# Optimization experiments

Measured on AMD Instinct MI355X. Metric: run time of the kernel, lower is better.

## Reference

```python
import jax, jax.numpy as jnp
import numpy as np

B, T, DP, DQ, DO = 128, 2048, 256, 256, 256


def setup_inputs() -> dict:
    key = jax.random.key(0)
    ks = jax.random.split(key, 10)
    return {
        "input_p": jax.random.normal(ks[0], (B, DP), dtype=jnp.float32),
        "mask_p": jnp.ones((B,), dtype=jnp.float32),
        "input_q": jax.random.normal(ks[1], (B, T, DQ), dtype=jnp.float32),
        "mask_q": jax.random.randint(ks[2], (B, T), 0, 2, dtype=jnp.int32),
        "h_tm1": jax.random.normal(ks[3], (B, DO), dtype=jnp.float32),
        # layer-0 parameters (depth == 0)
        "W_p_r": jax.random.normal(ks[4], (DO, DP + DO), dtype=jnp.float32) * 0.04,
        "b_p_r": jnp.zeros((DO,), dtype=jnp.float32),
        "W_q": jax.random.normal(ks[5], (DO, DQ), dtype=jnp.float32) * 0.05,
        "b_q": jnp.zeros((DO,), dtype=jnp.float32),
        "w": jax.random.normal(ks[6], (DO,), dtype=jnp.float32) * 0.05,
        "match_b": jnp.ones((1,), dtype=jnp.float32),
        "depth": 0,
    }


def masked_softmax(x, m, axis=-1):
    x = jnp.clip(x, -15.0, 15.0)
    x = x * m
    e_x = jnp.exp(x - jnp.max(x, axis=axis, keepdims=True))
    e_x = e_x * m
    return e_x / (jnp.sum(e_x, axis=axis, keepdims=True) + 1e-6)


def reference(input_p, mask_p, input_q, mask_q, h_tm1, W_p_r, b_p_r, W_q, b_q, w, match_b, depth):
    mq = mask_q.astype(jnp.float32)
    # G_p_r: [B, 1, DO]
    G_p_r = (jnp.concatenate([input_p, h_tm1], axis=-1) @ W_p_r.T + b_p_r)[:, None, :]
    # G_q: [B, T, DO]
    G_q = input_q @ W_q.T + b_q
    G = jnp.tanh(G_p_r + G_q)
    alpha = jnp.einsum("btd,d->bt", G, w) + match_b  # [B, T]
    alpha = masked_softmax(alpha, mq, axis=-1)
    z = jnp.einsum("bt,btd->bd", alpha, input_q)  # bmm context
    return jnp.concatenate([input_p, z], axis=1)  # [B, DP+DQ]
```

## Files before the change

### kernel.cpp

```cpp
#include <hip/hip_runtime.h>
#include <hip/hip_bf16.h>

typedef short short8 __attribute__((ext_vector_type(8)));
typedef float floatx4 __attribute__((ext_vector_type(4)));

constexpr int Bn = 128, Tn = 2048, DPn = 256, DQn = 256, DOn = 256;
constexpr int RCH = 32;
constexpr int NCH = Tn / RCH;

__device__ inline unsigned pk2(float x, float y) {
    __hip_bfloat162 h = __float22bfloat162_rn(make_float2(x, y));
    return *(unsigned*)&h;
}
__device__ inline float fast_tanh(float x) {
    float e = __expf(2.0f * x);
    return 1.0f - 2.0f / (e + 1.0f);
}

__global__ __launch_bounds__(256) void prep_kernel(const float* __restrict__ wq,
                                                   unsigned short* __restrict__ wqbf,
                                                   const float* __restrict__ input_p,
                                                   const float* __restrict__ h_tm1,
                                                   const float* __restrict__ Wpr,
                                                   const float* __restrict__ bpr,
                                                   const float* __restrict__ bq,
                                                   float* __restrict__ base) {
    __shared__ float v[512];
    __shared__ float ps[128];
    int tid = threadIdx.x;
    if (blockIdx.x < 64) {
        int idx = blockIdx.x * 256 + tid;
        float4 x = ((const float4*)wq)[idx];
        ((uint2*)wqbf)[idx] = make_uint2(pk2(x.x, x.y), pk2(x.z, x.w));
        return;
    }
    int bi = blockIdx.x - 64;
    int b = bi >> 1, half = bi & 1;
    v[tid]       = input_p[b * DPn + tid];
    v[256 + tid] = h_tm1[b * DOn + tid];
    __syncthreads();
    int dl = tid & 127, seg = tid >> 7;
    int d = half * 128 + dl;
    const float4* row = (const float4*)(Wpr + (size_t)d * 512 + seg * 256);
    const float4* vv  = (const float4*)(v + seg * 256);
    float acc = 0.f;
#pragma unroll 8
    for (int i = 0; i < 64; i++) {
        float4 r = row[i], x = vv[i];
        acc = fmaf(r.x, x.x, acc);
        acc = fmaf(r.y, x.y, acc);
        acc = fmaf(r.z, x.z, acc);
        acc = fmaf(r.w, x.w, acc);
    }
    if (seg) ps[dl] = acc;
    __syncthreads();
    if (!seg) base[b * DOn + d] = acc + ps[dl] + bpr[d] + bq[d];
}

__global__ __launch_bounds__(256, 4) void fused_kernel(const float* __restrict__ q,
                                                       const unsigned short* __restrict__ wqbf,
                                                       const float* __restrict__ base,
                                                       const float* __restrict__ wvec,
                                                       const float* __restrict__ matchb,
                                                       const int* __restrict__ maskq,
                                                       float* __restrict__ zpart,
                                                       float* __restrict__ spart,
                                                       float* __restrict__ mpart) {
    __shared__ __align__(16) float tile[RCH * 256];
    __shared__ __align__(16) float zp[4][256];
    __shared__ __align__(16) float partl[32][4];

    int b = blockIdx.y, c = blockIdx.x;
    int t0 = c * RCH;
    int tid = threadIdx.x;
    int w = tid >> 6, lane = tid & 63, l15 = lane & 15, quad = lane >> 4;
    char* tb = (char*)tile;
    float mb = matchb[0];

    {
        const float* qsrc = q + ((size_t)b * Tn + t0) * DQn;
#pragma unroll
        for (int i = 0; i < 8; i++) {
            int r = w * 8 + i;
            float4 x = *(const float4*)(qsrc + (size_t)r * DQn + lane * 4);
            *(float4*)(tb + r * 1024 + ((lane * 16) ^ ((r & 7) << 4))) = x;
        }
    }
    __syncthreads();

    short8 af[2][8];
    {
        int swz = (l15 & 7) << 4;
#pragma unroll
        for (int mt = 0; mt < 2; mt++) {
            const char* ab = tb + (mt * 16 + l15) * 1024;
#pragma unroll
            for (int ks = 0; ks < 8; ks++) {
                int cb = quad * 32 + ks * 128;
                float4 f0 = *(const float4*)(ab + (cb ^ swz));
                float4 f1 = *(const float4*)(ab + ((cb + 16) ^ swz));
                union { unsigned u[4]; short8 s; } cv;
                cv.u[0] = pk2(f0.x, f0.y);
                cv.u[1] = pk2(f0.z, f0.w);
                cv.u[2] = pk2(f1.x, f1.y);
                cv.u[3] = pk2(f1.z, f1.w);
                af[mt][ks] = cv.s;
            }
        }
    }
    float prow[2][4] = {{0.f, 0.f, 0.f, 0.f}, {0.f, 0.f, 0.f, 0.f}};
    {
        const unsigned short* bbase = wqbf + (size_t)(w * 64 + l15) * 256 + quad * 8;
#pragma unroll
        for (int nt = 0; nt < 4; nt++) {
            short8 bfr[8];
#pragma unroll
            for (int ks = 0; ks < 8; ks++)
                bfr[ks] = *(const short8*)(bbase + nt * 16 * 256 + ks * 32);
            int n = w * 64 + nt * 16 + l15;
            float bnv = base[b * DOn + n];
            float wnv = wvec[n];
#pragma unroll
            for (int mt = 0; mt < 2; mt++) {
                floatx4 acc = {0.f, 0.f, 0.f, 0.f};
#pragma unroll
                for (int ks = 0; ks < 8; ks++)
                    acc = __builtin_amdgcn_mfma_f32_16x16x32_bf16(af[mt][ks], bfr[ks], acc, 0, 0, 0);
#pragma unroll
                for (int rr = 0; rr < 4; rr++) {
                    float gg = fast_tanh(acc[rr] + bnv);
                    prow[mt][rr] = fmaf(gg, wnv, prow[mt][rr]);
                }
            }
        }
    }
#pragma unroll
    for (int off = 1; off < 16; off <<= 1)
#pragma unroll
        for (int mt = 0; mt < 2; mt++)
#pragma unroll
            for (int rr = 0; rr < 4; rr++) prow[mt][rr] += __shfl_xor(prow[mt][rr], off);
    if (l15 == 0) {
#pragma unroll
        for (int mt = 0; mt < 2; mt++)
#pragma unroll
            for (int rr = 0; rr < 4; rr++) partl[mt * 16 + quad * 4 + rr][w] = prow[mt][rr];
    }
    __syncthreads();

    float ew;
    {
        int t = lane & 31;
        float4 pl = *(const float4*)&partl[t][0];
        float lg = pl.x + pl.y + pl.z + pl.w + mb;
        float m = (float)maskq[(size_t)b * Tn + t0 + t];
        float x = fminf(fmaxf(lg, -15.f), 15.f) * m;
        ew = __expf(x - 15.f) * m;
        float xm = x, es = ew;
#pragma unroll
        for (int off = 1; off < 32; off <<= 1) {
            xm = fmaxf(xm, __shfl_xor(xm, off));
            es += __shfl_xor(es, off);
        }
        if (tid == 0) {
            mpart[b * NCH + c] = xm;
            spart[b * NCH + c] = es;
        }
    }

    {
        float a0 = 0.f, a1 = 0.f, a2 = 0.f, a3 = 0.f;
#pragma unroll
        for (int i = 0; i < 8; i++) {
            int r = w * 8 + i;
            float e = __shfl(ew, r);
            float4 x = *(const float4*)(tb + r * 1024 + ((lane * 16) ^ (i << 4)));
            a0 = fmaf(e, x.x, a0);
            a1 = fmaf(e, x.y, a1);
            a2 = fmaf(e, x.z, a2);
            a3 = fmaf(e, x.w, a3);
        }
        *(float4*)&zp[w][lane * 4] = make_float4(a0, a1, a2, a3);
    }
    __syncthreads();
    {
        float zs = zp[0][tid] + zp[1][tid] + zp[2][tid] + zp[3][tid];
        zpart[((size_t)b * NCH + c) * DQn + tid] = zs;
    }
}

__global__ __launch_bounds__(256) void final_kernel(const float* __restrict__ input_p,
                                                    const float* __restrict__ zpart,
                                                    const float* __restrict__ spart,
                                                    const float* __restrict__ mpart,
                                                    float* __restrict__ out) {
    int b = blockIdx.x, tid = threadIdx.x;
    float S = 0.f, mx = -1e30f;
#pragma unroll 8
    for (int c = 0; c < NCH; c++) {
        S += spart[b * NCH + c];
        mx = fmaxf(mx, mpart[b * NCH + c]);
    }
    float denom = S + 1e-6f * __expf(mx - 15.f);
    float inv = 1.0f / denom;
    float zs = 0.f;
#pragma unroll 8
    for (int c = 0; c < NCH; c++) zs += zpart[((size_t)b * NCH + c) * DQn + tid];
    out[(size_t)b * 512 + tid] = input_p[(size_t)b * DPn + tid];
    out[(size_t)b * 512 + 256 + tid] = zs * inv;
}

extern "C" void kernel_launch(void* const* d_in, const int* in_sizes, int n_in,
                              void* d_out, int out_size, void* d_ws, size_t ws_size,
                              hipStream_t stream) {
    const float* input_p = (const float*)d_in[0];
    const float* input_q = (const float*)d_in[2];
    const int*   mask_q  = (const int*)d_in[3];
    const float* h_tm1   = (const float*)d_in[4];
    const float* W_p_r   = (const float*)d_in[5];
    const float* b_p_r   = (const float*)d_in[6];
    const float* W_q     = (const float*)d_in[7];
    const float* b_q     = (const float*)d_in[8];
    const float* w       = (const float*)d_in[9];
    const float* match_b = (const float*)d_in[10];
    float* out = (float*)d_out;

    char* ws = (char*)d_ws;
    unsigned short* wqbf = (unsigned short*)ws;
    float* base  = (float*)(ws + 131072);
    float* zpart = (float*)(ws + 262144);
    float* spart = (float*)(ws + 262144 + 8388608);
    float* mpart = (float*)(ws + 262144 + 8388608 + 32768);

    prep_kernel<<<320, 256, 0, stream>>>(W_q, wqbf, input_p, h_tm1, W_p_r, b_p_r, b_q, base);
    fused_kernel<<<dim3(NCH, Bn), 256, 0, stream>>>(input_q, wqbf, base, w, match_b,
                                                    mask_q, zpart, spart, mpart);
    final_kernel<<<Bn, 256, 0, stream>>>(input_p, zpart, spart, mpart, out);
}
```

Baseline: 482.9 us.

## Double chunk rows, load Q tile via global_load_lds, hold W_q fragments in registers

Doubles the per-block time chunk from 32 to 64 rows, so each block keeps all 4×8 bf16 W_q fragments in registers and reuses them across four 16-row sub-tiles. The global-to-register-to-LDS copy of the Q tile is replaced by direct global_load_lds, and the MFMA operands are swapped so each lane accumulates a whole row's logit with fewer cross-lane shuffles. Partial buffers shrink because there are half as many chunks. In exchange the kernel uses more registers and LDS, occupancy drops to 2 blocks per SIMD group, and the grid has half as many blocks.

```diff
diff --git a/kernel.cpp b/kernel.cpp
--- a/kernel.cpp
+++ b/kernel.cpp
@@ -5,7 +5,7 @@
 typedef float floatx4 __attribute__((ext_vector_type(4)));
 
 constexpr int Bn = 128, Tn = 2048, DPn = 256, DQn = 256, DOn = 256;
-constexpr int RCH = 32;
+constexpr int RCH = 64;
 constexpr int NCH = Tn / RCH;
 
 __device__ inline unsigned pk2(float x, float y) {
@@ -15,6 +15,11 @@
 __device__ inline float fast_tanh(float x) {
     float e = __expf(2.0f * x);
     return 1.0f - 2.0f / (e + 1.0f);
+}
+__device__ inline void load_lds16(const void* g, void* l) {
+    __builtin_amdgcn_global_load_lds((const __attribute__((address_space(1))) unsigned int*)g,
+                                     (__attribute__((address_space(3))) unsigned int*)l,
+                                     16, 0, 0);
 }
 
 __global__ __launch_bounds__(256) void prep_kernel(const float* __restrict__ wq,
@@ -57,7 +62,7 @@
     if (!seg) base[b * DOn + d] = acc + ps[dl] + bpr[d] + bq[d];
 }
 
-__global__ __launch_bounds__(256, 4) void fused_kernel(const float* __restrict__ q,
+__global__ __launch_bounds__(256, 2) void fused_kernel(const float* __restrict__ q,
                                                        const unsigned short* __restrict__ wqbf,
                                                        const float* __restrict__ base,
                                                        const float* __restrict__ wvec,
@@ -68,97 +73,90 @@
                                                        float* __restrict__ mpart) {
     __shared__ __align__(16) float tile[RCH * 256];
     __shared__ __align__(16) float zp[4][256];
-    __shared__ __align__(16) float partl[32][4];
+    __shared__ __align__(16) float partl[4][16][8];
 
     int b = blockIdx.y, c = blockIdx.x;
     int t0 = c * RCH;
     int tid = threadIdx.x;
     int w = tid >> 6, lane = tid & 63, l15 = lane & 15, quad = lane >> 4;
     char* tb = (char*)tile;
+
+    {
+        const char* qsrc = (const char*)(q + ((size_t)b * Tn + t0) * DQn);
+        int lb = lane * 16;
+#pragma unroll
+        for (int i = 0; i < 16; i++) {
+            int r = w * 16 + i;
+            load_lds16(qsrc + (size_t)r * 1024 + (lb ^ ((i & 7) << 4)), tile + r * 256);
+        }
+    }
+
+    short8 bfr[4][8];
+    const unsigned short* bbase = wqbf + (size_t)(w * 64 + l15) * 256 + quad * 8;
+#pragma unroll
+    for (int nn = 0; nn < 4; nn++)
+#pragma unroll
+        for (int ks = 0; ks < 8; ks++)
+            bfr[nn][ks] = *(const short8*)(bbase + nn * 16 * 256 + ks * 32);
+    floatx4 bn4[4], wn4[4];
+#pragma unroll
+    for (int nn = 0; nn < 4; nn++) {
+        int n0 = w * 64 + nn * 16 + quad * 4;
+        bn4[nn] = *(const floatx4*)(base + b * DOn + n0);
+        wn4[nn] = *(const floatx4*)(wvec + n0);
+    }
     float mb = matchb[0];
-
-    {
-        const float* qsrc = q + ((size_t)b * Tn + t0) * DQn;
-#pragma unroll
-        for (int i = 0; i < 8; i++) {
-            int r = w * 8 + i;
-            float4 x = *(const float4*)(qsrc + (size_t)r * DQn + lane * 4);
-            *(float4*)(tb + r * 1024 + ((lane * 16) ^ ((r & 7) << 4))) = x;
-        }
-    }
-    __syncthreads();
-
-    short8 af[2][8];
-    {
-        int swz = (l15 & 7) << 4;
-#pragma unroll
-        for (int mt = 0; mt < 2; mt++) {
-            const char* ab = tb + (mt * 16 + l15) * 1024;
-#pragma unroll
-            for (int ks = 0; ks < 8; ks++) {
-                int cb = quad * 32 + ks * 128;
-                float4 f0 = *(const float4*)(ab + (cb ^ swz));
-                float4 f1 = *(const float4*)(ab + ((cb + 16) ^ swz));
-                union { unsigned u[4]; short8 s; } cv;
-                cv.u[0] = pk2(f0.x, f0.y);
-                cv.u[1] = pk2(f0.z, f0.w);
-                cv.u[2] = pk2(f1.x, f1.y);
-                cv.u[3] = pk2(f1.z, f1.w);
-                af[mt][ks] = cv.s;
+    float mk = (float)maskq[(size_t)b * Tn + t0 + lane];
+    __syncthreads();
+
+    float plog[4] = {0.f, 0.f, 0.f, 0.f};
+    int swz = (l15 & 7) << 4;
+#pragma unroll
+    for (int tt = 0; tt < 4; tt++) {
+        const char* ab = tb + (tt * 16 + l15) * 1024;
+        short8 af[8];
+#pragma unroll
+        for (int ks = 0; ks < 8; ks++) {
+            int cb = quad * 32 + ks * 128;
+            float4 f0 = *(const float4*)(ab + (cb ^ swz));
+            float4 f1 = *(const float4*)(ab + ((cb + 16) ^ swz));
+            union { unsigned u[4]; short8 s; } cv;
+            cv.u[0] = pk2(f0.x, f0.y);
+            cv.u[1] = pk2(f0.z, f0.w);
+            cv.u[2] = pk2(f1.x, f1.y);
+            cv.u[3] = pk2(f1.z, f1.w);
+            af[ks] = cv.s;
+        }
+#pragma unroll
+        for (int nn = 0; nn < 4; nn++) {
+            floatx4 acc = {0.f, 0.f, 0.f, 0.f};
+#pragma unroll
+            for (int ks = 0; ks < 8; ks++)
+                acc = __builtin_amdgcn_mfma_f32_16x16x32_bf16(bfr[nn][ks], af[ks], acc, 0, 0, 0);
+#pragma unroll
+            for (int rr = 0; rr < 4; rr++) {
+                float gg = fast_tanh(acc[rr] + bn4[nn][rr]);
+                plog[tt] = fmaf(gg, wn4[nn][rr], plog[tt]);
             }
         }
     }
-    float prow[2][4] = {{0.f, 0.f, 0.f, 0.f}, {0.f, 0.f, 0.f, 0.f}};
-    {
-        const unsigned short* bbase = wqbf + (size_t)(w * 64 + l15) * 256 + quad * 8;
-#pragma unroll
-        for (int nt = 0; nt < 4; nt++) {
-            short8 bfr[8];
-#pragma unroll
-            for (int ks = 0; ks < 8; ks++)
-                bfr[ks] = *(const short8*)(bbase + nt * 16 * 256 + ks * 32);
-            int n = w * 64 + nt * 16 + l15;
-            float bnv = base[b * DOn + n];
-            float wnv = wvec[n];
-#pragma unroll
-            for (int mt = 0; mt < 2; mt++) {
-                floatx4 acc = {0.f, 0.f, 0.f, 0.f};
-#pragma unroll
-                for (int ks = 0; ks < 8; ks++)
-                    acc = __builtin_amdgcn_mfma_f32_16x16x32_bf16(af[mt][ks], bfr[ks], acc, 0, 0, 0);
-#pragma unroll
-                for (int rr = 0; rr < 4; rr++) {
-                    float gg = fast_tanh(acc[rr] + bnv);
-                    prow[mt][rr] = fmaf(gg, wnv, prow[mt][rr]);
-                }
-            }
-        }
-    }
-#pragma unroll
-    for (int off = 1; off < 16; off <<= 1)
-#pragma unroll
-        for (int mt = 0; mt < 2; mt++)
-#pragma unroll
-            for (int rr = 0; rr < 4; rr++) prow[mt][rr] += __shfl_xor(prow[mt][rr], off);
-    if (l15 == 0) {
-#pragma unroll
-        for (int mt = 0; mt < 2; mt++)
-#pragma unroll
-            for (int rr = 0; rr < 4; rr++) partl[mt * 16 + quad * 4 + rr][w] = prow[mt][rr];
-    }
+#pragma unroll
+    for (int tt = 0; tt < 4; tt++) {
+        plog[tt] += __shfl_xor(plog[tt], 16);
+        plog[tt] += __shfl_xor(plog[tt], 32);
+    }
+    partl[quad][l15][w] = plog[quad];
     __syncthreads();
 
     float ew;
     {
-        int t = lane & 31;
-        float4 pl = *(const float4*)&partl[t][0];
-        float lg = pl.x + pl.y + pl.z + pl.w + mb;
-        float m = (float)maskq[(size_t)b * Tn + t0 + t];
-        float x = fminf(fmaxf(lg, -15.f), 15.f) * m;
-        ew = __expf(x - 15.f) * m;
+        floatx4 pl = *(const floatx4*)&partl[lane >> 4][l15][0];
+        float lg = pl[0] + pl[1] + pl[2] + pl[3] + mb;
+        float x = fminf(fmaxf(lg, -15.f), 15.f) * mk;
+        ew = __expf(x - 15.f) * mk;
         float xm = x, es = ew;
 #pragma unroll
-        for (int off = 1; off < 32; off <<= 1) {
+        for (int off = 1; off < 64; off <<= 1) {
             xm = fmaxf(xm, __shfl_xor(xm, off));
             es += __shfl_xor(es, off);
         }
@@ -171,10 +169,10 @@
     {
         float a0 = 0.f, a1 = 0.f, a2 = 0.f, a3 = 0.f;
 #pragma unroll
-        for (int i = 0; i < 8; i++) {
-            int r = w * 8 + i;
+        for (int i = 0; i < 16; i++) {
+            int r = w * 16 + i;
             float e = __shfl(ew, r);
-            float4 x = *(const float4*)(tb + r * 1024 + ((lane * 16) ^ (i << 4)));
+            float4 x = *(const float4*)(tb + r * 1024 + ((lane * 16) ^ ((i & 7) << 4)));
             a0 = fmaf(e, x.x, a0);
             a1 = fmaf(e, x.y, a1);
             a2 = fmaf(e, x.z, a2);
@@ -229,8 +227,8 @@
     unsigned short* wqbf = (unsigned short*)ws;
     float* base  = (float*)(ws + 131072);
     float* zpart = (float*)(ws + 262144);
-    float* spart = (float*)(ws + 262144 + 8388608);
-    float* mpart = (float*)(ws + 262144 + 8388608 + 32768);
+    float* spart = (float*)(ws + 262144 + 4194304);
+    float* mpart = (float*)(ws + 262144 + 4194304 + 16384);
 
     prep_kernel<<<320, 256, 0, stream>>>(W_q, wqbf, input_p, h_tm1, W_p_r, b_p_r, b_q, base);
     fused_kernel<<<dim3(NCH, Bn), 256, 0, stream>>>(input_q, wqbf, base, w, match_b,
```

New measurement: 490.0 us. No clear change (+1.5%).
